# Kernel tuning notes

Measured on AMD Instinct MI355X. Metric: run time of the kernel, lower is better.

Reference implementation:

```python
import jax, jax.numpy as jnp
import numpy as np

MASK_VALUE = -1000000.0


def setup_inputs() -> dict:
    key = jax.random.key(0)
    k1, k2, k3, k4 = jax.random.split(key, 4)
    B, Lq, Lk, d = 32, 1024, 1024, 128
    return {
        "query": jax.random.normal(k1, (B, Lq, d), dtype=jnp.float32),
        "key": jax.random.normal(k2, (B, Lk, d), dtype=jnp.float32),
        "value": jax.random.normal(k3, (B, Lk, d), dtype=jnp.float32),
        "valid_length": jax.random.randint(k4, (B,), 0, Lk, dtype=jnp.int64),
    }


def reference(query, key, value, valid_length):
    # query [B, Lq, d], key/value [B, Lk, d], valid_length [B]
    d = query.shape[-1]
    # scores [B, Lq, Lk]
    scores = jnp.einsum("bqd,bkd->bqk", query, key) / jnp.sqrt(jnp.float32(d))
    Lk = key.shape[1]
    # mask positions >= valid_length with -1e6 (per-batch, broadcast over Lq)
    pos = jnp.arange(Lk)  # [Lk]
    mask = pos[None, None, :] >= valid_length[:, None, None]  # [B, 1, Lk]
    scores = jnp.where(mask, MASK_VALUE, scores)
    attn = jax.nn.softmax(scores, axis=-1)
    # dropout p=0.0 in eval -> identity
    return jnp.einsum("bqk,bkd->bqd", attn, value)
```

## Files before the change

### kernel.cpp

```cpp
#include <hip/hip_runtime.h>

#define B_N 32
#define LQ  1024
#define LK  1024
#define DH  128

typedef __attribute__((ext_vector_type(4))) float    f32x4;
typedef __attribute__((ext_vector_type(8))) short    s16x8;
typedef __attribute__((ext_vector_type(4))) _Float16 f16x4;
typedef __attribute__((ext_vector_type(8))) _Float16 f16x8;

__device__ inline unsigned short f2bf(float f) {
    union { float f; unsigned u; } c; c.f = f;
    unsigned u = c.u;
    u += 0x7fffu + ((u >> 16) & 1u);
    return (unsigned short)(u >> 16);
}

#define ESCALE 0.12751743f

#define G2L16(gp, lp) __builtin_amdgcn_global_load_lds(                         \
    (const __attribute__((address_space(1))) void*)(gp),                        \
    (__attribute__((address_space(3))) void*)(lp), 16, 0, 0)

__global__ __launch_bounds__(256)
void prep_kv(const float* __restrict__ K, const float* __restrict__ V,
             const int* __restrict__ VL,
             unsigned short* __restrict__ Kb, _Float16* __restrict__ Vt)
{
    __shared__ float tl[32 * 132];
    const int tid  = threadIdx.x;
    const int lane = tid & 63;
    const int wv   = tid >> 6;
    const int n    = lane & 15;
    const int quad = lane >> 4;

    const int  idx = blockIdx.x;
    const bool isK = (idx >> 10) == 0;
    const int  b   = (idx & 7) | (((idx >> 3) & 3) << 3);
    const int  kt  = (idx >> 5) & 31;

    const int vl = VL[b];
    if (isK) {
        if (vl <= 0 || kt >= 2 * ((vl + 63) >> 6)) return;
    } else {
        const int nch = (vl > 0) ? ((vl + 63) >> 6) : 16;
        if (kt >= 2 * nch) return;
    }

    const float4* src = (const float4*)((isK ? K : V) + ((size_t)b * LK + kt * 32) * DH);
    #pragma unroll
    for (int h = 0; h < 4; ++h) {
        const int i2 = h * 256 + tid;
        const int row = i2 >> 5, c4 = i2 & 31;
        *(float4*)&tl[row * 132 + c4 * 4] = src[i2];
    }
    __syncthreads();

    if (isK) {
        union { s16x8 v; unsigned short u[8]; } t8;
        #pragma unroll
        for (int h = 0; h < 2; ++h) {
            const int f = wv * 2 + h;
            const int tt2 = f >> 2, s = f & 3;
            const float* p = &tl[(tt2 * 16 + n) * 132 + s * 32 + quad * 8];
            const float4 a = *(const float4*)p;
            const float4 c = *(const float4*)(p + 4);
            t8.u[0] = f2bf(a.x); t8.u[1] = f2bf(a.y); t8.u[2] = f2bf(a.z); t8.u[3] = f2bf(a.w);
            t8.u[4] = f2bf(c.x); t8.u[5] = f2bf(c.y); t8.u[6] = f2bf(c.z); t8.u[7] = f2bf(c.w);
            const int w = b * 256 + (kt * 2 + tt2) * 4 + s;
            *(s16x8*)(Kb + (size_t)w * 512 + lane * 8) = t8.v;
        }
    } else {
        #pragma unroll
        for (int h = 0; h < 2; ++h) {
            const int f  = wv * 2 + h;
            const int kg = f >> 2, dp = f & 3;
            f16x8 t8;
            #pragma unroll
            for (int i = 0; i < 4; ++i) {
                const float* row = &tl[(kg * 16 + quad * 4 + i) * 132 + dp * 32 + n];
                t8[i]     = (_Float16)row[0];
                t8[4 + i] = (_Float16)row[16];
            }
            const int v = (b * 64 + kt * 2 + kg) * 4 + dp;
            *(f16x8*)(Vt + (size_t)v * 512 + lane * 8) = t8;
        }
    }
}

__global__ __launch_bounds__(128)
void attn_fwd(const float* __restrict__ Q, const unsigned short* __restrict__ Kb,
              const _Float16* __restrict__ Vt, const int* __restrict__ VL,
              float* __restrict__ O)
{
    __shared__ __align__(16) unsigned short bufK[2][16 * 512];
    __shared__ __align__(16) _Float16       bufV[2][16 * 512];

    const int tid  = threadIdx.x;
    const int lane = tid & 63;
    const int w    = tid >> 6;
    const int quad = lane >> 4;
    const int m16  = lane & 15;

    const int idx = blockIdx.x;
    const int qg  = (idx >> 5) & 15;
    const int b   = (idx & 7) | ((((idx >> 3) + (idx >> 8)) & 3) << 3);
    const int q0  = qg * 64;

    const int vl  = VL[b];
    const int nch = (vl > 0) ? ((vl + 63) >> 6) : 16;
    const float emaskval = (vl == 0) ? 1.0f : 0.0f;

    s16x8 qf[2][4];
    #pragma unroll
    for (int h = 0; h < 2; ++h) {
        const float* qrow = Q + ((size_t)b * LQ + q0 + w * 32 + h * 16 + m16) * DH + quad * 8;
        #pragma unroll
        for (int s = 0; s < 4; ++s) {
            const float4 a = *(const float4*)(qrow + s * 32);
            const float4 c = *(const float4*)(qrow + s * 32 + 4);
            union { s16x8 v; unsigned short u[8]; } t;
            t.u[0] = f2bf(a.x); t.u[1] = f2bf(a.y); t.u[2] = f2bf(a.z); t.u[3] = f2bf(a.w);
            t.u[4] = f2bf(c.x); t.u[5] = f2bf(c.y); t.u[6] = f2bf(c.z); t.u[7] = f2bf(c.w);
            qf[h][s] = t.v;
        }
    }

    f32x4 o[2][8];
    #pragma unroll
    for (int h = 0; h < 2; ++h)
        #pragma unroll
        for (int dt = 0; dt < 8; ++dt) o[h][dt] = (f32x4){0.f, 0.f, 0.f, 0.f};
    float lrun[2] = {0.f, 0.f};

    const unsigned short* kg0 = Kb + (size_t)b * (256 * 512);
    const _Float16*       vg0 = Vt + (size_t)b * (256 * 512);
    const int co = tid * 8;

#define STAGE(c, t)                                                             \
    do {                                                                        \
        const unsigned short* gk_ = kg0 + (size_t)(t) * 8192;                   \
        const _Float16*       gv_ = vg0 + (size_t)(t) * 8192;                   \
        _Pragma("unroll")                                                       \
        for (int it_ = 0; it_ < 8; ++it_)                                       \
            G2L16(gk_ + it_ * 1024 + co, &bufK[c][it_ * 1024 + co]);            \
        _Pragma("unroll")                                                       \
        for (int it_ = 0; it_ < 8; ++it_)                                       \
            G2L16(gv_ + it_ * 1024 + co, &bufV[c][it_ * 1024 + co]);            \
    } while (0)

    STAGE(0, 0);
    asm volatile("s_waitcnt vmcnt(0)" ::: "memory");
    __builtin_amdgcn_sched_barrier(0);
    __builtin_amdgcn_s_barrier();

    int cur = 0;
    for (int t = 0; t < nch; ++t) {
        if (t + 1 < nch) STAGE(cur ^ 1, t + 1);

        const unsigned short* bk = &bufK[cur][0];
        const _Float16*       bv = &bufV[cur][0];
        const bool maskc = (t * 64 + 64 > vl);
        f16x4 pA[2][4];

        #pragma unroll
        for (int g = 0; g < 4; ++g) {
            f32x4 st0 = (f32x4){0.f, 0.f, 0.f, 0.f};
            f32x4 st1 = (f32x4){0.f, 0.f, 0.f, 0.f};
            #pragma unroll
            for (int s = 0; s < 4; ++s) {
                const s16x8 kf = *(const s16x8*)(bk + (g * 4 + s) * 512 + lane * 8);
                st0 = __builtin_amdgcn_mfma_f32_16x16x32_bf16(kf, qf[0][s], st0, 0, 0, 0);
                st1 = __builtin_amdgcn_mfma_f32_16x16x32_bf16(kf, qf[1][s], st1, 0, 0, 0);
            }
            #pragma unroll
            for (int i = 0; i < 4; ++i) {
                float e0 = __builtin_amdgcn_exp2f(st0[i] * ESCALE);
                float e1 = __builtin_amdgcn_exp2f(st1[i] * ESCALE);
                if (maskc && (t * 64 + g * 16 + quad * 4 + i >= vl)) { e0 = emaskval; e1 = emaskval; }
                lrun[0] += e0; lrun[1] += e1;
                pA[0][g][i] = (_Float16)e0;
                pA[1][g][i] = (_Float16)e1;
            }
        }

        #pragma unroll
        for (int g = 0; g < 4; ++g) {
            #pragma unroll
            for (int dp = 0; dp < 4; ++dp) {
                const f16x8 w8 = *(const f16x8*)(bv + (g * 4 + dp) * 512 + lane * 8);
                const f16x4 lo = __builtin_shufflevector(w8, w8, 0, 1, 2, 3);
                const f16x4 hi = __builtin_shufflevector(w8, w8, 4, 5, 6, 7);
                o[0][dp * 2]     = __builtin_amdgcn_mfma_f32_16x16x16f16(pA[0][g], lo, o[0][dp * 2],     0, 0, 0);
                o[0][dp * 2 + 1] = __builtin_amdgcn_mfma_f32_16x16x16f16(pA[0][g], hi, o[0][dp * 2 + 1], 0, 0, 0);
                o[1][dp * 2]     = __builtin_amdgcn_mfma_f32_16x16x16f16(pA[1][g], lo, o[1][dp * 2],     0, 0, 0);
                o[1][dp * 2 + 1] = __builtin_amdgcn_mfma_f32_16x16x16f16(pA[1][g], hi, o[1][dp * 2 + 1], 0, 0, 0);
            }
        }

        asm volatile("s_waitcnt vmcnt(0)" ::: "memory");
        __builtin_amdgcn_sched_barrier(0);
        __builtin_amdgcn_s_barrier();
        cur ^= 1;
    }
#undef STAGE

    #pragma unroll
    for (int h = 0; h < 2; ++h) {
        float L = lrun[h];
        L += __shfl_xor(L, 16);
        L += __shfl_xor(L, 32);
        const size_t obase = ((size_t)b * LQ + q0 + w * 32 + h * 16 + quad * 4) * DH + m16;
        #pragma unroll
        for (int r = 0; r < 4; ++r) {
            const float inv = 1.0f / __shfl(L, quad * 4 + r);
            #pragma unroll
            for (int dt = 0; dt < 8; ++dt)
                O[obase + (size_t)r * DH + dt * 16] = o[h][dt][r] * inv;
        }
    }
}

extern "C" void kernel_launch(void* const* d_in, const int* in_sizes, int n_in,
                              void* d_out, int out_size, void* d_ws, size_t ws_size,
                              hipStream_t stream) {
    const float* Q  = (const float*)d_in[0];
    const float* K  = (const float*)d_in[1];
    const float* V  = (const float*)d_in[2];
    const int*   VL = (const int*)d_in[3];
    float* O = (float*)d_out;
    (void)in_sizes; (void)n_in; (void)out_size; (void)ws_size;

    unsigned short* Kb = (unsigned short*)d_ws;
    _Float16*       Vt = (_Float16*)(Kb + (size_t)B_N * 256 * 512);

    prep_kv<<<dim3(2048), dim3(256), 0, stream>>>(K, V, VL, Kb, Vt);
    attn_fwd<<<dim3(B_N * (LQ / 64)), dim3(128), 0, stream>>>(Q, Kb, Vt, VL, O);
}
```

Measured before the change: 121.6 us.

## Split KV chunks across two wave pairs and reduce partial outputs in LDS

Doubles the block to 256 threads: each pair of waves covers the same 32 query rows, and the two pairs alternate over even and odd KV chunks. Loads are prefetched two chunks ahead into double buffers, with a partial vmcnt wait in place of a full drain. At the end, one wave pair writes its partial O accumulators and row sums to LDS, and the other pair adds them in and normalizes. This is meant to hide load latency and increase in-flight work per CU, at the cost of an extra barrier per chunk, idle waves on half the chunks, and the reduction epilogue.

Result: slower. 126.2 us (+3.8%).

```diff
diff --git a/kernel.cpp b/kernel.cpp
--- a/kernel.cpp
+++ b/kernel.cpp
@@ -89,7 +89,7 @@
     }
 }
 
-__global__ __launch_bounds__(128)
+__global__ __launch_bounds__(256)
 void attn_fwd(const float* __restrict__ Q, const unsigned short* __restrict__ Kb,
               const _Float16* __restrict__ Vt, const int* __restrict__ VL,
               float* __restrict__ O)
@@ -99,7 +99,9 @@
 
     const int tid  = threadIdx.x;
     const int lane = tid & 63;
-    const int w    = tid >> 6;
+    const int wv   = tid >> 6;
+    const int h2   = wv >> 1;
+    const int j    = wv & 1;
     const int quad = lane >> 4;
     const int m16  = lane & 15;
 
@@ -115,7 +117,7 @@
     s16x8 qf[2][4];
     #pragma unroll
     for (int h = 0; h < 2; ++h) {
-        const float* qrow = Q + ((size_t)b * LQ + q0 + w * 32 + h * 16 + m16) * DH + quad * 8;
+        const float* qrow = Q + ((size_t)b * LQ + q0 + h2 * 32 + h * 16 + m16) * DH + quad * 8;
         #pragma unroll
         for (int s = 0; s < 4; ++s) {
             const float4 a = *(const float4*)(qrow + s * 32);
@@ -143,81 +145,102 @@
         const unsigned short* gk_ = kg0 + (size_t)(t) * 8192;                   \
         const _Float16*       gv_ = vg0 + (size_t)(t) * 8192;                   \
         _Pragma("unroll")                                                       \
-        for (int it_ = 0; it_ < 8; ++it_)                                       \
-            G2L16(gk_ + it_ * 1024 + co, &bufK[c][it_ * 1024 + co]);            \
+        for (int it_ = 0; it_ < 4; ++it_)                                       \
+            G2L16(gk_ + it_ * 2048 + co, &bufK[c][it_ * 2048 + co]);            \
         _Pragma("unroll")                                                       \
-        for (int it_ = 0; it_ < 8; ++it_)                                       \
-            G2L16(gv_ + it_ * 1024 + co, &bufV[c][it_ * 1024 + co]);            \
+        for (int it_ = 0; it_ < 4; ++it_)                                       \
+            G2L16(gv_ + it_ * 2048 + co, &bufV[c][it_ * 2048 + co]);            \
     } while (0)
 
     STAGE(0, 0);
-    asm volatile("s_waitcnt vmcnt(0)" ::: "memory");
-    __builtin_amdgcn_sched_barrier(0);
-    __builtin_amdgcn_s_barrier();
-
-    int cur = 0;
+    STAGE(1, 1);
+
     for (int t = 0; t < nch; ++t) {
-        if (t + 1 < nch) STAGE(cur ^ 1, t + 1);
-
-        const unsigned short* bk = &bufK[cur][0];
-        const _Float16*       bv = &bufV[cur][0];
-        const bool maskc = (t * 64 + 64 > vl);
-        f16x4 pA[2][4];
-
-        #pragma unroll
-        for (int g = 0; g < 4; ++g) {
-            f32x4 st0 = (f32x4){0.f, 0.f, 0.f, 0.f};
-            f32x4 st1 = (f32x4){0.f, 0.f, 0.f, 0.f};
-            #pragma unroll
-            for (int s = 0; s < 4; ++s) {
-                const s16x8 kf = *(const s16x8*)(bk + (g * 4 + s) * 512 + lane * 8);
-                st0 = __builtin_amdgcn_mfma_f32_16x16x32_bf16(kf, qf[0][s], st0, 0, 0, 0);
-                st1 = __builtin_amdgcn_mfma_f32_16x16x32_bf16(kf, qf[1][s], st1, 0, 0, 0);
-            }
-            #pragma unroll
-            for (int i = 0; i < 4; ++i) {
-                float e0 = __builtin_amdgcn_exp2f(st0[i] * ESCALE);
-                float e1 = __builtin_amdgcn_exp2f(st1[i] * ESCALE);
-                if (maskc && (t * 64 + g * 16 + quad * 4 + i >= vl)) { e0 = emaskval; e1 = emaskval; }
-                lrun[0] += e0; lrun[1] += e1;
-                pA[0][g][i] = (_Float16)e0;
-                pA[1][g][i] = (_Float16)e1;
-            }
-        }
-
-        #pragma unroll
-        for (int g = 0; g < 4; ++g) {
-            #pragma unroll
-            for (int dp = 0; dp < 4; ++dp) {
-                const f16x8 w8 = *(const f16x8*)(bv + (g * 4 + dp) * 512 + lane * 8);
-                const f16x4 lo = __builtin_shufflevector(w8, w8, 0, 1, 2, 3);
-                const f16x4 hi = __builtin_shufflevector(w8, w8, 4, 5, 6, 7);
-                o[0][dp * 2]     = __builtin_amdgcn_mfma_f32_16x16x16f16(pA[0][g], lo, o[0][dp * 2],     0, 0, 0);
-                o[0][dp * 2 + 1] = __builtin_amdgcn_mfma_f32_16x16x16f16(pA[0][g], hi, o[0][dp * 2 + 1], 0, 0, 0);
-                o[1][dp * 2]     = __builtin_amdgcn_mfma_f32_16x16x16f16(pA[1][g], lo, o[1][dp * 2],     0, 0, 0);
-                o[1][dp * 2 + 1] = __builtin_amdgcn_mfma_f32_16x16x16f16(pA[1][g], hi, o[1][dp * 2 + 1], 0, 0, 0);
-            }
-        }
-
-        asm volatile("s_waitcnt vmcnt(0)" ::: "memory");
+        if (t + 1 < nch) { asm volatile("s_waitcnt vmcnt(8)" ::: "memory"); }
+        else             { asm volatile("s_waitcnt vmcnt(0)" ::: "memory"); }
         __builtin_amdgcn_sched_barrier(0);
         __builtin_amdgcn_s_barrier();
-        cur ^= 1;
+        __builtin_amdgcn_sched_barrier(0);
+
+        if ((t & 1) == j) {
+            const unsigned short* bk = &bufK[t & 1][0];
+            const _Float16*       bv = &bufV[t & 1][0];
+            const bool maskc = (t * 64 + 64 > vl);
+            f16x4 pA[2][4];
+
+            #pragma unroll
+            for (int g = 0; g < 4; ++g) {
+                f32x4 st0 = (f32x4){0.f, 0.f, 0.f, 0.f};
+                f32x4 st1 = (f32x4){0.f, 0.f, 0.f, 0.f};
+                #pragma unroll
+                for (int s = 0; s < 4; ++s) {
+                    const s16x8 kf = *(const s16x8*)(bk + (g * 4 + s) * 512 + lane * 8);
+                    st0 = __builtin_amdgcn_mfma_f32_16x16x32_bf16(kf, qf[0][s], st0, 0, 0, 0);
+                    st1 = __builtin_amdgcn_mfma_f32_16x16x32_bf16(kf, qf[1][s], st1, 0, 0, 0);
+                }
+                #pragma unroll
+                for (int i = 0; i < 4; ++i) {
+                    float e0 = __builtin_amdgcn_exp2f(st0[i] * ESCALE);
+                    float e1 = __builtin_amdgcn_exp2f(st1[i] * ESCALE);
+                    if (maskc && (t * 64 + g * 16 + quad * 4 + i >= vl)) { e0 = emaskval; e1 = emaskval; }
+                    lrun[0] += e0; lrun[1] += e1;
+                    pA[0][g][i] = (_Float16)e0;
+                    pA[1][g][i] = (_Float16)e1;
+                }
+            }
+
+            #pragma unroll
+            for (int g = 0; g < 4; ++g) {
+                #pragma unroll
+                for (int dp = 0; dp < 4; ++dp) {
+                    const f16x8 w8 = *(const f16x8*)(bv + (g * 4 + dp) * 512 + lane * 8);
+                    const f16x4 lo = __builtin_shufflevector(w8, w8, 0, 1, 2, 3);
+                    const f16x4 hi = __builtin_shufflevector(w8, w8, 4, 5, 6, 7);
+                    o[0][dp * 2]     = __builtin_amdgcn_mfma_f32_16x16x16f16(pA[0][g], lo, o[0][dp * 2],     0, 0, 0);
+                    o[0][dp * 2 + 1] = __builtin_amdgcn_mfma_f32_16x16x16f16(pA[0][g], hi, o[0][dp * 2 + 1], 0, 0, 0);
+                    o[1][dp * 2]     = __builtin_amdgcn_mfma_f32_16x16x16f16(pA[1][g], lo, o[1][dp * 2],     0, 0, 0);
+                    o[1][dp * 2 + 1] = __builtin_amdgcn_mfma_f32_16x16x16f16(pA[1][g], hi, o[1][dp * 2 + 1], 0, 0, 0);
+                }
+            }
+        }
+
+        __builtin_amdgcn_s_barrier();
+        __builtin_amdgcn_sched_barrier(0);
+        if (t + 2 < nch) STAGE(t & 1, t + 2);
     }
 #undef STAGE
 
-    #pragma unroll
-    for (int h = 0; h < 2; ++h) {
-        float L = lrun[h];
-        L += __shfl_xor(L, 16);
-        L += __shfl_xor(L, 32);
-        const size_t obase = ((size_t)b * LQ + q0 + w * 32 + h * 16 + quad * 4) * DH + m16;
-        #pragma unroll
-        for (int r = 0; r < 4; ++r) {
-            const float inv = 1.0f / __shfl(L, quad * 4 + r);
+    f32x4* Om = (f32x4*)&bufK[0][0];
+    float*  Lm = (float*)&bufV[0][0];
+    if (j == 1) {
+        #pragma unroll
+        for (int h = 0; h < 2; ++h) {
             #pragma unroll
             for (int dt = 0; dt < 8; ++dt)
-                O[obase + (size_t)r * DH + dt * 16] = o[h][dt][r] * inv;
+                Om[((h2 * 2 + h) * 8 + dt) * 64 + lane] = o[h][dt];
+            Lm[(h2 * 2 + h) * 64 + lane] = lrun[h];
+        }
+    }
+    __syncthreads();
+    if (j == 0) {
+        #pragma unroll
+        for (int h = 0; h < 2; ++h) {
+            f32x4 om[8];
+            #pragma unroll
+            for (int dt = 0; dt < 8; ++dt)
+                om[dt] = o[h][dt] + Om[((h2 * 2 + h) * 8 + dt) * 64 + lane];
+            float L = lrun[h] + Lm[(h2 * 2 + h) * 64 + lane];
+
+            L += __shfl_xor(L, 16);
+            L += __shfl_xor(L, 32);
+            const size_t obase = ((size_t)b * LQ + q0 + h2 * 32 + h * 16 + quad * 4) * DH + m16;
+            #pragma unroll
+            for (int r = 0; r < 4; ++r) {
+                const float inv = 1.0f / __shfl(L, quad * 4 + r);
+                #pragma unroll
+                for (int dt = 0; dt < 8; ++dt)
+                    O[obase + (size_t)r * DH + dt * 16] = om[dt][r] * inv;
+            }
         }
     }
 }
@@ -236,5 +259,5 @@
     _Float16*       Vt = (_Float16*)(Kb + (size_t)B_N * 256 * 512);
 
     prep_kv<<<dim3(2048), dim3(256), 0, stream>>>(K, V, VL, Kb, Vt);
-    attn_fwd<<<dim3(B_N * (LQ / 64)), dim3(128), 0, stream>>>(Q, Kb, Vt, VL, O);
-}
+    attn_fwd<<<dim3(B_N * (LQ / 64)), dim3(256), 0, stream>>>(Q, Kb, Vt, VL, O);
+}
```
